# Kernel tuning notes

Hardware: AMD Instinct MI355X
Metric: run time of the kernel (lower is better)

## Reference

```python
import jax, jax.numpy as jnp
import numpy as np
import math

MEM_DIM = 256   # channel dim of each memory slot
FEA_DIM = 1000  # number of memory slots (softmax axis)


def setup_inputs() -> dict:
    key = jax.random.key(0)
    kx, kw = jax.random.split(key)
    x = jax.random.normal(kx, (32, 64, 64, MEM_DIM), dtype=jnp.float32)
    std = 1.0 / math.sqrt(FEA_DIM)
    weight = jax.random.uniform(kw, (FEA_DIM, MEM_DIM), dtype=jnp.float32,
                                minval=-std, maxval=std)
    return {"x": x, "weight": weight}


def reference(x, weight):
    B, H, W, C = x.shape            # C == mem_dim
    xf = x.reshape(-1, C)           # [N, C], N = B*H*W
    # distance = inputs @ weight^T -> [N, fea_dim]
    dist = jnp.einsum('nc,fc->nf', xf, weight)
    att = jax.nn.softmax(dist, axis=1)          # [N, fea_dim]
    out = jnp.einsum('nf,fc->nc', att, weight)  # [N, C]
    out = out.reshape(B, H, W, C)
    # entropy: reshape att to [B, H*W*fea_dim], mean(-a*log a) per sample
    a = att.reshape(B, -1)
    ent = jnp.mean(-a * jnp.log(a), axis=-1, keepdims=True)  # [B, 1]
    return out, ent
```

## Files before the change

### kernel.cpp

```cpp
#include <hip/hip_runtime.h>
#include <stdint.h>

typedef unsigned int u32;
typedef unsigned short u16;
typedef u32 u32x4 __attribute__((ext_vector_type(4)));
typedef float f32x4 __attribute__((ext_vector_type(4)));

#define MEM_DIM 256
#define FEA 1000
#define FPAD 1024
#define BM 128
#define NIT 32
#define NOUT 33554432

__device__ __forceinline__ u16 f2bf(float x) {
  u32 u = __builtin_bit_cast(u32, x);
  u32 r = (u + 0x7fffu + ((u >> 16) & 1u)) >> 16;
  return (u16)r;
}

__device__ __forceinline__ u32 cvtpk(float lo, float hi) {
  u32 d;
  asm("v_cvt_pk_bf16_f32 %0, %1, %2" : "=v"(d) : "v"(lo), "v"(hi));
  return d;
}

__device__ __forceinline__ void mfma16(f32x4& acc, u32x4 a, u32x4 b) {
  asm("v_mfma_f32_16x16x32_bf16 %0, %1, %2, %0" : "+v"(acc) : "v"(a), "v"(b));
}

#define GLOAD_LDS16(gp, lp) __builtin_amdgcn_global_load_lds( \
    (const __attribute__((address_space(1))) u32*)(gp),       \
    (__attribute__((address_space(3))) u32*)(lp), 16, 0, 0)

__global__ void prep_kernel(const float* __restrict__ W, u16* __restrict__ Wswz,
                            u16* __restrict__ Wt, float* __restrict__ entpart) {
  int f = blockIdx.x;
  int c = threadIdx.x;
  float v = (f < FEA) ? W[f * MEM_DIM + c] : 0.0f;
  u16 b = f2bf(v);
  Wswz[f * MEM_DIM + (c ^ ((f & 7) << 3))] = b;
  Wt[c * FPAD + (f ^ (((c >> 1) & 3) << 3))] = b;
  if (blockIdx.x < 4) entpart[blockIdx.x * 256 + threadIdx.x] = 0.0f;
}

__global__ __launch_bounds__(256, 2) void fused_kernel(
    const float* __restrict__ X, const u16* __restrict__ Wswz,
    const u16* __restrict__ Wt, float* __restrict__ Out,
    float* __restrict__ entpart) {
  __shared__ __attribute__((aligned(16))) char smem[65536];
  __shared__ float entw[4];
  const int tid = threadIdx.x;
  const int wave = tid >> 6;
  const int lane = tid & 63;
  const int g = lane >> 4;
  const int q = lane & 15;
  const long rowbase = (long)blockIdx.x * BM + wave * 32;

  u32x4 xf[2][8];
#pragma unroll
  for (int ms = 0; ms < 2; ++ms) {
    const float* xr = X + (rowbase + ms * 16 + q) * MEM_DIM;
#pragma unroll
    for (int kk = 0; kk < 8; ++kk) {
      const f32x4* p = (const f32x4*)(xr + kk * 32 + g * 8);
      f32x4 a = p[0], b = p[1];
      u32x4 v;
      v.x = cvtpk(a.x, a.y); v.y = cvtpk(a.z, a.w);
      v.z = cvtpk(b.x, b.y); v.w = cvtpk(b.z, b.w);
      xf[ms][kk] = v;
    }
  }

  const char* WswzB = (const char*)Wswz;
  const char* WtB = (const char*)Wt;
  auto stage = [&](int it, int buf) {
#pragma unroll
    for (int jj = 0; jj < 4; ++jj) {
      int j = wave * 4 + jj;
      GLOAD_LDS16(WswzB + (size_t)it * 16384 + j * 1024 + lane * 16,
                  smem + buf * 16384 + j * 1024);
    }
#pragma unroll
    for (int jj = 0; jj < 4; ++jj) {
      int j = wave * 4 + jj;
      GLOAD_LDS16(WtB + (size_t)it * 64 + (size_t)(16 * j + (lane >> 2)) * 2048
                      + (lane & 3) * 16,
                  smem + 32768 + buf * 16384 + j * 1024);
    }
  };

  f32x4 ot[16][2];
  f32x4 z4 = {0.f, 0.f, 0.f, 0.f};
#pragma unroll
  for (int i = 0; i < 16; ++i) { ot[i][0] = z4; ot[i][1] = z4; }
  float zz[2] = {0.f, 0.f}, tt[2] = {0.f, 0.f};

  stage(0, 0);
  asm volatile("s_waitcnt vmcnt(0)" ::: "memory");
  __syncthreads();

  for (int it = 0; it < NIT; ++it) {
    const int cur = it & 1;
    if (it + 1 < NIT) stage(it + 1, cur ^ 1);
    const char* wb = smem + cur * 16384;
    const char* wt = smem + 32768 + cur * 16384;

    f32x4 st[2][2];
    st[0][0] = z4; st[0][1] = z4; st[1][0] = z4; st[1][1] = z4;
#pragma unroll
    for (int kk = 0; kk < 8; ++kk) {
#pragma unroll
      for (int fs = 0; fs < 2; ++fs) {
        const int fl = fs * 16 + q;
        const int off = fl * 512 + ((kk * 64 + g * 16) ^ ((fl & 7) << 4));
        u32x4 wfrag = *(const u32x4*)(wb + off);
        mfma16(st[fs][0], wfrag, xf[0][kk]);
        mfma16(st[fs][1], wfrag, xf[1][kk]);
      }
    }

    u32 pw[2][2][2];
#pragma unroll
    for (int fs = 0; fs < 2; ++fs) {
#pragma unroll
      for (int ms = 0; ms < 2; ++ms) {
        float s0 = st[fs][ms][0], s1 = st[fs][ms][1];
        float s2 = st[fs][ms][2], s3 = st[fs][ms][3];
        float p0 = __expf(s0), p1 = __expf(s1);
        float p2 = __expf(s2), p3 = __expf(s3);
        zz[ms] += (p0 + p1) + (p2 + p3);
        tt[ms] += (p0 * s0 + p1 * s1) + (p2 * s2 + p3 * s3);
        pw[fs][ms][0] = cvtpk(p0, p1);
        pw[fs][ms][1] = cvtpk(p2, p3);
      }
    }

    u32x4 pfrag[2];
#pragma unroll
    for (int ms = 0; ms < 2; ++ms) {
      u32 wd[4];
#pragma unroll
      for (int w = 0; w < 4; ++w) {
        int src = ((2 * (g & 1) + (w >> 1)) << 4) | q;
        u32 v0 = (u32)__shfl((int)pw[0][ms][w & 1], src, 64);
        u32 v1 = (u32)__shfl((int)pw[1][ms][w & 1], src, 64);
        wd[w] = (g >= 2) ? v1 : v0;
      }
      u32x4 pf; pf.x = wd[0]; pf.y = wd[1]; pf.z = wd[2]; pf.w = wd[3];
      pfrag[ms] = pf;
    }

#pragma unroll
    for (int ct = 0; ct < 16; ++ct) {
      const int off = ct * 1024 + q * 64 + ((g << 4) ^ (((q >> 1) & 3) << 4));
      u32x4 wtfrag = *(const u32x4*)(wt + off);
      mfma16(ot[ct][0], wtfrag, pfrag[0]);
      mfma16(ot[ct][1], wtfrag, pfrag[1]);
    }

    asm volatile("s_waitcnt vmcnt(0)" ::: "memory");
    __syncthreads();
  }

#pragma unroll
  for (int ms = 0; ms < 2; ++ms) {
    zz[ms] += __shfl_xor(zz[ms], 16, 64);
    zz[ms] += __shfl_xor(zz[ms], 32, 64);
    tt[ms] += __shfl_xor(tt[ms], 16, 64);
    tt[ms] += __shfl_xor(tt[ms], 32, 64);
    zz[ms] -= 24.0f;
  }

  float er = 0.0f;
#pragma unroll
  for (int ms = 0; ms < 2; ++ms) er += __logf(zz[ms]) - tt[ms] / zz[ms];
#pragma unroll
  for (int d = 1; d < 64; d <<= 1) er += __shfl_xor(er, d, 64);
  if (lane == 0) entw[wave] = er * 0.25f;

#pragma unroll
  for (int ms = 0; ms < 2; ++ms) {
    float rz = 1.0f / zz[ms];
    float* orow = Out + (rowbase + ms * 16 + q) * MEM_DIM;
#pragma unroll
    for (int ct = 0; ct < 16; ++ct) {
      f32x4 v = ot[ct][ms] * rz;
      *(f32x4*)(orow + ct * 16 + g * 4) = v;
    }
  }

  __syncthreads();
  if (tid == 0) entpart[blockIdx.x] = entw[0] + entw[1] + entw[2] + entw[3];
}

__global__ void ent_final(const float* __restrict__ entpart,
                          float* __restrict__ entout) {
  int b = blockIdx.x;
  int l = threadIdx.x;
  float v = (l < 32) ? entpart[b * 32 + l] : 0.0f;
#pragma unroll
  for (int d = 1; d < 64; d <<= 1) v += __shfl_xor(v, d, 64);
  if (l == 0) entout[b] = v * (1.0f / 4096000.0f);
}

extern "C" void kernel_launch(void* const* d_in, const int* in_sizes, int n_in,
                              void* d_out, int out_size, void* d_ws, size_t ws_size,
                              hipStream_t stream) {
  (void)in_sizes; (void)n_in; (void)out_size;
  const float* X = (const float*)d_in[0];
  const float* W = (const float*)d_in[1];
  float* Out = (float*)d_out;
  u16* Wswz = (u16*)d_ws;
  u16* Wt = (u16*)((char*)d_ws + 524288);
  float* entpart = (float*)((char*)d_ws + 1048576);
  if (ws_size < 1048576 + 4096) return;
  prep_kernel<<<dim3(1024), dim3(256), 0, stream>>>(W, Wswz, Wt, entpart);
  fused_kernel<<<dim3(1024), dim3(256), 0, stream>>>(X, Wswz, Wt, Out, entpart);
  ent_final<<<dim3(32), dim3(64), 0, stream>>>(entpart, Out + NOUT);
}
```

Before: 186.4 us.

## Double rows per block to 256 and keep output accumulators in AGPRs

Each wave now handles 64 rows instead of 32, so every W fragment read from LDS feeds four MFMAs instead of two. The number of blocks drops to 512 and launch bounds go to one block per SIMD group. The output accumulators, now twice as large, are placed in accumulation registers through a new MFMA variant with an AGPR constraint. The intent is to halve the per-row traffic for W staging and LDS reads. The cost is lower occupancy, higher register pressure and fewer blocks to cover the 256 CUs.

```diff
diff --git a/kernel.cpp b/kernel.cpp
--- a/kernel.cpp
+++ b/kernel.cpp
@@ -9,7 +9,7 @@
 #define MEM_DIM 256
 #define FEA 1000
 #define FPAD 1024
-#define BM 128
+#define BM 256
 #define NIT 32
 #define NOUT 33554432
 
@@ -27,6 +27,9 @@
 
 __device__ __forceinline__ void mfma16(f32x4& acc, u32x4 a, u32x4 b) {
   asm("v_mfma_f32_16x16x32_bf16 %0, %1, %2, %0" : "+v"(acc) : "v"(a), "v"(b));
+}
+__device__ __forceinline__ void mfma16a(f32x4& acc, u32x4 a, u32x4 b) {
+  asm("v_mfma_f32_16x16x32_bf16 %0, %1, %2, %0" : "+a"(acc) : "v"(a), "v"(b));
 }
 
 #define GLOAD_LDS16(gp, lp) __builtin_amdgcn_global_load_lds( \
@@ -41,10 +44,10 @@
   u16 b = f2bf(v);
   Wswz[f * MEM_DIM + (c ^ ((f & 7) << 3))] = b;
   Wt[c * FPAD + (f ^ (((c >> 1) & 3) << 3))] = b;
-  if (blockIdx.x < 4) entpart[blockIdx.x * 256 + threadIdx.x] = 0.0f;
-}
-
-__global__ __launch_bounds__(256, 2) void fused_kernel(
+  if (blockIdx.x < 2) entpart[blockIdx.x * 256 + threadIdx.x] = 0.0f;
+}
+
+__global__ __launch_bounds__(256, 1) void fused_kernel(
     const float* __restrict__ X, const u16* __restrict__ Wswz,
     const u16* __restrict__ Wt, float* __restrict__ Out,
     float* __restrict__ entpart) {
@@ -55,11 +58,11 @@
   const int lane = tid & 63;
   const int g = lane >> 4;
   const int q = lane & 15;
-  const long rowbase = (long)blockIdx.x * BM + wave * 32;
-
-  u32x4 xf[2][8];
-#pragma unroll
-  for (int ms = 0; ms < 2; ++ms) {
+  const long rowbase = (long)blockIdx.x * BM + wave * 64;
+
+  u32x4 xf[4][8];
+#pragma unroll
+  for (int ms = 0; ms < 4; ++ms) {
     const float* xr = X + (rowbase + ms * 16 + q) * MEM_DIM;
 #pragma unroll
     for (int kk = 0; kk < 8; ++kk) {
@@ -90,11 +93,13 @@
     }
   };
 
-  f32x4 ot[16][2];
+  f32x4 ot[16][4];
   f32x4 z4 = {0.f, 0.f, 0.f, 0.f};
 #pragma unroll
-  for (int i = 0; i < 16; ++i) { ot[i][0] = z4; ot[i][1] = z4; }
-  float zz[2] = {0.f, 0.f}, tt[2] = {0.f, 0.f};
+  for (int i = 0; i < 16; ++i)
+#pragma unroll
+    for (int ms = 0; ms < 4; ++ms) ot[i][ms] = z4;
+  float zz[4] = {0.f, 0.f, 0.f, 0.f}, tt[4] = {0.f, 0.f, 0.f, 0.f};
 
   stage(0, 0);
   asm volatile("s_waitcnt vmcnt(0)" ::: "memory");
@@ -106,8 +111,11 @@
     const char* wb = smem + cur * 16384;
     const char* wt = smem + 32768 + cur * 16384;
 
-    f32x4 st[2][2];
-    st[0][0] = z4; st[0][1] = z4; st[1][0] = z4; st[1][1] = z4;
+    f32x4 st[2][4];
+#pragma unroll
+    for (int fs = 0; fs < 2; ++fs)
+#pragma unroll
+      for (int ms = 0; ms < 4; ++ms) st[fs][ms] = z4;
 #pragma unroll
     for (int kk = 0; kk < 8; ++kk) {
 #pragma unroll
@@ -117,34 +125,32 @@
         u32x4 wfrag = *(const u32x4*)(wb + off);
         mfma16(st[fs][0], wfrag, xf[0][kk]);
         mfma16(st[fs][1], wfrag, xf[1][kk]);
+        mfma16(st[fs][2], wfrag, xf[2][kk]);
+        mfma16(st[fs][3], wfrag, xf[3][kk]);
       }
     }
 
-    u32 pw[2][2][2];
-#pragma unroll
-    for (int fs = 0; fs < 2; ++fs) {
-#pragma unroll
-      for (int ms = 0; ms < 2; ++ms) {
+    u32x4 pfrag[4];
+#pragma unroll
+    for (int ms = 0; ms < 4; ++ms) {
+      u32 pw[2][2];
+#pragma unroll
+      for (int fs = 0; fs < 2; ++fs) {
         float s0 = st[fs][ms][0], s1 = st[fs][ms][1];
         float s2 = st[fs][ms][2], s3 = st[fs][ms][3];
         float p0 = __expf(s0), p1 = __expf(s1);
         float p2 = __expf(s2), p3 = __expf(s3);
         zz[ms] += (p0 + p1) + (p2 + p3);
         tt[ms] += (p0 * s0 + p1 * s1) + (p2 * s2 + p3 * s3);
-        pw[fs][ms][0] = cvtpk(p0, p1);
-        pw[fs][ms][1] = cvtpk(p2, p3);
+        pw[fs][0] = cvtpk(p0, p1);
+        pw[fs][1] = cvtpk(p2, p3);
       }
-    }
-
-    u32x4 pfrag[2];
-#pragma unroll
-    for (int ms = 0; ms < 2; ++ms) {
       u32 wd[4];
 #pragma unroll
       for (int w = 0; w < 4; ++w) {
         int src = ((2 * (g & 1) + (w >> 1)) << 4) | q;
-        u32 v0 = (u32)__shfl((int)pw[0][ms][w & 1], src, 64);
-        u32 v1 = (u32)__shfl((int)pw[1][ms][w & 1], src, 64);
+        u32 v0 = (u32)__shfl((int)pw[0][w & 1], src, 64);
+        u32 v1 = (u32)__shfl((int)pw[1][w & 1], src, 64);
         wd[w] = (g >= 2) ? v1 : v0;
       }
       u32x4 pf; pf.x = wd[0]; pf.y = wd[1]; pf.z = wd[2]; pf.w = wd[3];
@@ -155,8 +161,10 @@
     for (int ct = 0; ct < 16; ++ct) {
       const int off = ct * 1024 + q * 64 + ((g << 4) ^ (((q >> 1) & 3) << 4));
       u32x4 wtfrag = *(const u32x4*)(wt + off);
-      mfma16(ot[ct][0], wtfrag, pfrag[0]);
-      mfma16(ot[ct][1], wtfrag, pfrag[1]);
+      mfma16a(ot[ct][0], wtfrag, pfrag[0]);
+      mfma16a(ot[ct][1], wtfrag, pfrag[1]);
+      mfma16a(ot[ct][2], wtfrag, pfrag[2]);
+      mfma16a(ot[ct][3], wtfrag, pfrag[3]);
     }
 
     asm volatile("s_waitcnt vmcnt(0)" ::: "memory");
@@ -164,7 +172,7 @@
   }
 
 #pragma unroll
-  for (int ms = 0; ms < 2; ++ms) {
+  for (int ms = 0; ms < 4; ++ms) {
     zz[ms] += __shfl_xor(zz[ms], 16, 64);
     zz[ms] += __shfl_xor(zz[ms], 32, 64);
     tt[ms] += __shfl_xor(tt[ms], 16, 64);
@@ -174,13 +182,13 @@
 
   float er = 0.0f;
 #pragma unroll
-  for (int ms = 0; ms < 2; ++ms) er += __logf(zz[ms]) - tt[ms] / zz[ms];
+  for (int ms = 0; ms < 4; ++ms) er += __logf(zz[ms]) - tt[ms] / zz[ms];
 #pragma unroll
   for (int d = 1; d < 64; d <<= 1) er += __shfl_xor(er, d, 64);
   if (lane == 0) entw[wave] = er * 0.25f;
 
 #pragma unroll
-  for (int ms = 0; ms < 2; ++ms) {
+  for (int ms = 0; ms < 4; ++ms) {
     float rz = 1.0f / zz[ms];
     float* orow = Out + (rowbase + ms * 16 + q) * MEM_DIM;
 #pragma unroll
@@ -198,7 +206,7 @@
                           float* __restrict__ entout) {
   int b = blockIdx.x;
   int l = threadIdx.x;
-  float v = (l < 32) ? entpart[b * 32 + l] : 0.0f;
+  float v = (l < 16) ? entpart[b * 16 + l] : 0.0f;
 #pragma unroll
   for (int d = 1; d < 64; d <<= 1) v += __shfl_xor(v, d, 64);
   if (l == 0) entout[b] = v * (1.0f / 4096000.0f);
@@ -216,6 +224,6 @@
   float* entpart = (float*)((char*)d_ws + 1048576);
   if (ws_size < 1048576 + 4096) return;
   prep_kernel<<<dim3(1024), dim3(256), 0, stream>>>(W, Wswz, Wt, entpart);
-  fused_kernel<<<dim3(1024), dim3(256), 0, stream>>>(X, Wswz, Wt, Out, entpart);
+  fused_kernel<<<dim3(512), dim3(256), 0, stream>>>(X, Wswz, Wt, Out, entpart);
   ent_final<<<dim3(32), dim3(64), 0, stream>>>(entpart, Out + NOUT);
 }
```

Result: slower. 205.2 us (+10.1%).
